# Performance work log

Hardware: AMD Instinct MI355X
Metric: run time of the kernel (lower is better)

## Reference

```python
import jax, jax.numpy as jnp
from jax import lax
import numpy as np

B, L, H, T = 64, 512, 768, 9


def setup_inputs() -> dict:
    key = jax.random.key(0)
    ks = jax.random.split(key, 6)
    hidden = jax.random.normal(ks[0], (B, L, H), dtype=jnp.float32)
    attention_mask = jnp.ones((B, L), dtype=jnp.int32)
    labels = jax.random.randint(ks[1], (B, L), 0, T).astype(jnp.int64)
    W = jax.random.normal(ks[2], (H, T), dtype=jnp.float32) * 0.02
    b = jnp.zeros((T,), dtype=jnp.float32)
    start_trans = jax.random.normal(ks[3], (T,), dtype=jnp.float32) * 0.1
    end_trans = jax.random.normal(ks[4], (T,), dtype=jnp.float32) * 0.1
    trans = jax.random.normal(ks[5], (T, T), dtype=jnp.float32) * 0.1
    return {"hidden": hidden, "attention_mask": attention_mask, "labels": labels,
            "W": W, "b": b, "start_trans": start_trans, "end_trans": end_trans, "trans": trans}


def _crf_nll(logits, safe_labels, mask, start_trans, end_trans, trans):
    # torchcrf: llh = numerator(path score) - denominator(log partition); loss = -mean(llh)
    maskf = mask.astype(logits.dtype)  # [B,L]
    # ---- numerator (gold path score) ----
    first_tags = safe_labels[:, 0]  # [B]
    num = start_trans[first_tags] + jnp.take_along_axis(logits[:, 0], first_tags[:, None], axis=1)[:, 0]
    emit = jnp.take_along_axis(logits, safe_labels[..., None], axis=2)[..., 0]  # [B,L]
    step_trans = trans[safe_labels[:, :-1], safe_labels[:, 1:]]  # [B,L-1]
    num = num + jnp.sum((step_trans + emit[:, 1:]) * maskf[:, 1:], axis=1)
    seq_ends = mask.sum(axis=1).astype(jnp.int32) - 1  # [B]
    last_tags = jnp.take_along_axis(safe_labels, seq_ends[:, None], axis=1)[:, 0]
    num = num + end_trans[last_tags]
    # ---- denominator (forward algorithm, logsumexp recurrence) ----
    def step(score, inp):
        e_t, m_t = inp  # [B,T], [B] bool
        # broadcast: score[b,i] + trans[i,j] + e_t[b,j]
        nxt = jax.nn.logsumexp(score[:, :, None] + trans[None, :, :] + e_t[:, None, :], axis=1)
        score = jnp.where(m_t[:, None], nxt, score)
        return score, None

    init = start_trans[None, :] + logits[:, 0]  # [B,T]
    xs = (jnp.swapaxes(logits[:, 1:], 0, 1), jnp.swapaxes(mask[:, 1:], 0, 1))
    final, _ = lax.scan(step, init, xs)
    denom = jax.nn.logsumexp(final + end_trans[None, :], axis=1)  # [B]
    llh = num - denom
    return -jnp.mean(llh)


def reference(hidden, attention_mask, labels, W, b, start_trans, end_trans, trans):
    logits = hidden @ W + b  # [B,L,T]
    mask = attention_mask.astype(bool)
    safe_labels = jnp.where(labels == -100, 0, labels)
    loss = _crf_nll(logits, safe_labels, mask, start_trans, end_trans, trans)
    return loss, logits
```

## Files before the change

### kernel.cpp

```cpp
#include <hip/hip_runtime.h>
#include <hip/hip_bf16.h>

#define NB 64
#define NL 512
#define NH 768
#define NT 9

#define LOG2E 1.4426950408889634f
#define LN2   0.6931471805599453f
#define NEG_INF -1e30f

#if defined(__has_builtin)
#if __has_builtin(__builtin_amdgcn_exp2f)
#define EXP2F(x) __builtin_amdgcn_exp2f(x)
#else
#define EXP2F(x) exp2f(x)
#endif
#if __has_builtin(__builtin_amdgcn_logf)
#define LOG2F(x) __builtin_amdgcn_logf(x)
#else
#define LOG2F(x) log2f(x)
#endif
#else
#define EXP2F(x) exp2f(x)
#define LOG2F(x) log2f(x)
#endif

__global__ __launch_bounds__(256) void gemm_kernel(
    const float* __restrict__ hidden, const float* __restrict__ W,
    const float* __restrict__ bias, float* __restrict__ out)
{
  __shared__ __align__(16) float w_lds[4 * 192 * 12];
  const int tid = threadIdx.x;
  for (int idx = tid; idx < NH * NT; idx += 256) {
    int k = idx / NT;
    int j = idx - k * NT;
    w_lds[(k & 3) * 2304 + (k >> 2) * 12 + j] = W[idx];
  }
  if (blockIdx.x == 0 && tid == 0) out[0] = 0.0f;
  __syncthreads();

  const int lane = tid & 63;
  const int wave = tid >> 6;
  const int gw = blockIdx.x * 4 + wave;
  const float bj = (lane < NT) ? bias[lane] : 0.0f;

  for (int row = gw; row < NB * NL; row += 4096) {
    const float4* hp = reinterpret_cast<const float4*>(hidden + (size_t)row * NH);
    float acc[NT];
#pragma unroll
    for (int j = 0; j < NT; ++j) acc[j] = 0.0f;
#pragma unroll
    for (int i = 0; i < 3; ++i) {
      const int kk = lane + 64 * i;
      const float4 h4 = hp[kk];
#pragma unroll
      for (int m = 0; m < 4; ++m) {
        const float hh = (m == 0) ? h4.x : (m == 1) ? h4.y : (m == 2) ? h4.z : h4.w;
        const float* wl = &w_lds[m * 2304 + kk * 12];
        const float4 wa = *reinterpret_cast<const float4*>(wl);
        const float4 wb = *reinterpret_cast<const float4*>(wl + 4);
        const float w8 = wl[8];
        acc[0] = fmaf(hh, wa.x, acc[0]);
        acc[1] = fmaf(hh, wa.y, acc[1]);
        acc[2] = fmaf(hh, wa.z, acc[2]);
        acc[3] = fmaf(hh, wa.w, acc[3]);
        acc[4] = fmaf(hh, wb.x, acc[4]);
        acc[5] = fmaf(hh, wb.y, acc[5]);
        acc[6] = fmaf(hh, wb.z, acc[6]);
        acc[7] = fmaf(hh, wb.w, acc[7]);
        acc[8] = fmaf(hh, w8, acc[8]);
      }
    }
#pragma unroll
    for (int off = 32; off >= 1; off >>= 1) {
#pragma unroll
      for (int j = 0; j < NT; ++j) acc[j] += __shfl_xor(acc[j], off);
    }
    float v = acc[0];
#pragma unroll
    for (int j = 1; j < NT; ++j)
      if (lane == j) v = acc[j];
    if (lane < NT) out[1 + (size_t)row * NT + lane] = v + bj;
  }
}

#define NC 32
#define CS 16

__global__ __launch_bounds__(576) void crf_kernel(
    const float* __restrict__ logits,
    const int* __restrict__ mask, const int* __restrict__ labels,
    const float* __restrict__ start_trans, const float* __restrict__ end_trans,
    const float* __restrict__ trans, float* __restrict__ loss_out)
{
  const int b = blockIdx.x;
  const int tid = threadIdx.x;

  __shared__ float lg[NL * NT];
  __shared__ float trans_s[NT * NT];
  __shared__ float E_s[NT * NT];
  __shared__ int mask_s[NL];
  __shared__ float P[NC * NT * NT];
  __shared__ float red_num[9];
  __shared__ float red_cnt[9];

  const float* lgg = logits + (size_t)b * NL * NT;
  for (int idx = tid; idx < NL * NT; idx += 576) lg[idx] = lgg[idx];
  if (tid < NT * NT) {
    float tv = trans[tid];
    trans_s[tid] = tv;
    E_s[tid] = EXP2F(tv * LOG2E);
  }
  if (tid < NL) mask_s[tid] = mask[b * NL + tid];
  __syncthreads();

  float numpart = 0.0f, cntpart = 0.0f;
  if (tid < NL) {
    int lab = labels[b * NL + tid];
    if (lab == -100) lab = 0;
    if (tid == 0) {
      numpart = start_trans[lab] + lg[lab];
    } else {
      int labp = labels[b * NL + tid - 1];
      if (labp == -100) labp = 0;
      float mf = (float)mask_s[tid];
      numpart = mf * (trans_s[labp * NT + lab] + lg[tid * NT + lab]);
    }
    cntpart = (float)mask_s[tid];
  }
#pragma unroll
  for (int off = 32; off >= 1; off >>= 1) {
    numpart += __shfl_down(numpart, off);
    cntpart += __shfl_down(cntpart, off);
  }
  if ((tid & 63) == 0) {
    red_num[tid >> 6] = numpart;
    red_cnt[tid >> 6] = cntpart;
  }

  if (tid < NC * NT) {
    const int c = tid / NT;
    const int i = tid - c * NT;
    float Er[NT * NT];
#pragma unroll
    for (int kj = 0; kj < NT * NT; ++kj) Er[kj] = E_s[kj];
    float run[NT];
    const int t0 = 1 + CS * c;
    if (mask_s[t0]) {
#pragma unroll
      for (int j = 0; j < NT; ++j) run[j] = trans_s[i * NT + j] + lg[t0 * NT + j];
    } else {
#pragma unroll
      for (int j = 0; j < NT; ++j) run[j] = (i == j) ? 0.0f : NEG_INF;
    }
    const int tend = min(t0 + CS, NL);
    for (int t = t0 + 1; t < tend; ++t) {
      if (!mask_s[t]) continue;
      float m = run[0];
#pragma unroll
      for (int k = 1; k < NT; ++k) m = fmaxf(m, run[k]);
      float p[NT];
#pragma unroll
      for (int k = 0; k < NT; ++k) p[k] = EXP2F((run[k] - m) * LOG2E);
      float dot[NT];
#pragma unroll
      for (int j = 0; j < NT; ++j) dot[j] = 0.0f;
#pragma unroll
      for (int k = 0; k < NT; ++k) {
#pragma unroll
        for (int j = 0; j < NT; ++j) dot[j] = fmaf(p[k], Er[k * NT + j], dot[j]);
      }
#pragma unroll
      for (int j = 0; j < NT; ++j)
        run[j] = fmaf(LOG2F(dot[j]), LN2, m) + lg[t * NT + j];
    }
#pragma unroll
    for (int j = 0; j < NT; ++j) P[c * (NT * NT) + i * NT + j] = run[j];
  }
  __syncthreads();

  if (tid < 64) {
    const int j = tid;
    const int jj = (j < NT) ? j : 0;
    float v = (j < NT) ? (start_trans[j] + lg[j]) : NEG_INF;
    for (int c = 0; c < NC; ++c) {
      float s[NT];
#pragma unroll
      for (int i = 0; i < NT; ++i)
        s[i] = __shfl(v, i) + P[c * (NT * NT) + i * NT + jj];
      float m = s[0];
#pragma unroll
      for (int i = 1; i < NT; ++i) m = fmaxf(m, s[i]);
      float sum = 0.0f;
#pragma unroll
      for (int i = 0; i < NT; ++i) sum += EXP2F((s[i] - m) * LOG2E);
      v = fmaf(LOG2F(sum), LN2, m);
    }
    float x = (j < NT) ? (v + end_trans[j]) : NEG_INF;
    float m = x;
#pragma unroll
    for (int off = 32; off >= 1; off >>= 1) m = fmaxf(m, __shfl_xor(m, off));
    float e = (j < NT) ? EXP2F((x - m) * LOG2E) : 0.0f;
#pragma unroll
    for (int off = 32; off >= 1; off >>= 1) e += __shfl_xor(e, off);
    if (tid == 0) {
      float denom = fmaf(LOG2F(e), LN2, m);
      float num = 0.0f, cnt = 0.0f;
#pragma unroll
      for (int w = 0; w < 9; ++w) {
        num += red_num[w];
        cnt += red_cnt[w];
      }
      int seq_end = (int)cnt - 1;
      int lastlab = labels[b * NL + seq_end];
      if (lastlab == -100) lastlab = 0;
      num += end_trans[lastlab];
      float llh = num - denom;
      atomicAdd(loss_out, -llh * (1.0f / NB));
    }
  }
}

extern "C" void kernel_launch(void* const* d_in, const int* in_sizes, int n_in,
                              void* d_out, int out_size, void* d_ws, size_t ws_size,
                              hipStream_t stream) {
  const float* hidden      = (const float*)d_in[0];
  const int*   attn_mask   = (const int*)d_in[1];
  const int*   labels      = (const int*)d_in[2];
  const float* W           = (const float*)d_in[3];
  const float* bias        = (const float*)d_in[4];
  const float* start_trans = (const float*)d_in[5];
  const float* end_trans   = (const float*)d_in[6];
  const float* trans       = (const float*)d_in[7];
  float* out = (float*)d_out;

  hipLaunchKernelGGL(gemm_kernel, dim3(1024), dim3(256), 0, stream,
                     hidden, W, bias, out);
  hipLaunchKernelGGL(crf_kernel, dim3(64), dim3(576), 0, stream,
                     out + 1, attn_mask, labels, start_trans, end_trans, trans, out);
}
```

Before: 187.3 us.

## Cache W in registers, process two rows per wave, vectorize CRF logits load

The GEMM kernel now preloads each lane's slice of W into 108 registers and processes two hidden rows per wave iteration, splitting the final cross-lane reduction so the two half-waves finish different rows. This removes repeated LDS reads of W and halves the shuffle-reduction cost per row. Logits are also written to an aligned workspace so the CRF kernel can load them with float4 vector loads instead of unaligned scalar loads. The large register footprint may lower occupancy, and the extra workspace store adds write traffic.

New measurement: 189.0 us. No clear change (+0.9%).

```diff
diff --git a/kernel.cpp b/kernel.cpp
--- a/kernel.cpp
+++ b/kernel.cpp
@@ -28,60 +28,86 @@
 
 __global__ __launch_bounds__(256) void gemm_kernel(
     const float* __restrict__ hidden, const float* __restrict__ W,
-    const float* __restrict__ bias, float* __restrict__ out)
+    const float* __restrict__ bias, float* __restrict__ out,
+    float* __restrict__ ws)
 {
-  __shared__ __align__(16) float w_lds[4 * 192 * 12];
+  __shared__ __align__(16) float w_lds[NH * NT];
   const int tid = threadIdx.x;
-  for (int idx = tid; idx < NH * NT; idx += 256) {
-    int k = idx / NT;
-    int j = idx - k * NT;
-    w_lds[(k & 3) * 2304 + (k >> 2) * 12 + j] = W[idx];
-  }
+  for (int idx = tid; idx < NH * NT / 4; idx += 256)
+    reinterpret_cast<float4*>(w_lds)[idx] = reinterpret_cast<const float4*>(W)[idx];
   if (blockIdx.x == 0 && tid == 0) out[0] = 0.0f;
   __syncthreads();
 
   const int lane = tid & 63;
-  const int wave = tid >> 6;
-  const int gw = blockIdx.x * 4 + wave;
-  const float bj = (lane < NT) ? bias[lane] : 0.0f;
-
-  for (int row = gw; row < NB * NL; row += 4096) {
-    const float4* hp = reinterpret_cast<const float4*>(hidden + (size_t)row * NH);
-    float acc[NT];
-#pragma unroll
-    for (int j = 0; j < NT; ++j) acc[j] = 0.0f;
+  const int wv = blockIdx.x * 4 + (tid >> 6);
+  const int jj = (lane < 32) ? lane : lane - 32;
+  const float bx = (jj < NT) ? bias[jj] : 0.0f;
+
+  float wreg[3][4][NT];
+#pragma unroll
+  for (int i = 0; i < 3; ++i) {
+#pragma unroll
+    for (int m = 0; m < 4; ++m) {
+      const float* wl = &w_lds[(4 * (lane + 64 * i) + m) * NT];
+#pragma unroll
+      for (int j = 0; j < NT; ++j) wreg[i][m][j] = wl[j];
+    }
+  }
+
+  for (int p = wv; p < NB * NL / 2; p += 4096) {
+    const float4* hp0 = reinterpret_cast<const float4*>(hidden + (size_t)(2 * p) * NH);
+    const float4* hp1 = reinterpret_cast<const float4*>(hidden + (size_t)(2 * p + 1) * NH);
+    float4 a[3], b[3];
+#pragma unroll
+    for (int i = 0; i < 3; ++i) a[i] = hp0[lane + 64 * i];
+#pragma unroll
+    for (int i = 0; i < 3; ++i) b[i] = hp1[lane + 64 * i];
+
+    float acc0[NT], acc1[NT];
+#pragma unroll
+    for (int j = 0; j < NT; ++j) { acc0[j] = 0.0f; acc1[j] = 0.0f; }
 #pragma unroll
     for (int i = 0; i < 3; ++i) {
-      const int kk = lane + 64 * i;
-      const float4 h4 = hp[kk];
 #pragma unroll
       for (int m = 0; m < 4; ++m) {
-        const float hh = (m == 0) ? h4.x : (m == 1) ? h4.y : (m == 2) ? h4.z : h4.w;
-        const float* wl = &w_lds[m * 2304 + kk * 12];
-        const float4 wa = *reinterpret_cast<const float4*>(wl);
-        const float4 wb = *reinterpret_cast<const float4*>(wl + 4);
-        const float w8 = wl[8];
-        acc[0] = fmaf(hh, wa.x, acc[0]);
-        acc[1] = fmaf(hh, wa.y, acc[1]);
-        acc[2] = fmaf(hh, wa.z, acc[2]);
-        acc[3] = fmaf(hh, wa.w, acc[3]);
-        acc[4] = fmaf(hh, wb.x, acc[4]);
-        acc[5] = fmaf(hh, wb.y, acc[5]);
-        acc[6] = fmaf(hh, wb.z, acc[6]);
-        acc[7] = fmaf(hh, wb.w, acc[7]);
-        acc[8] = fmaf(hh, w8, acc[8]);
-      }
-    }
-#pragma unroll
-    for (int off = 32; off >= 1; off >>= 1) {
-#pragma unroll
-      for (int j = 0; j < NT; ++j) acc[j] += __shfl_xor(acc[j], off);
-    }
-    float v = acc[0];
+        const float ha = (m == 0) ? a[i].x : (m == 1) ? a[i].y : (m == 2) ? a[i].z : a[i].w;
+        const float hb = (m == 0) ? b[i].x : (m == 1) ? b[i].y : (m == 2) ? b[i].z : b[i].w;
+#pragma unroll
+        for (int j = 0; j < NT; ++j) {
+          acc0[j] = fmaf(ha, wreg[i][m][j], acc0[j]);
+          acc1[j] = fmaf(hb, wreg[i][m][j], acc1[j]);
+        }
+      }
+    }
+#pragma unroll
+    for (int off = 1; off <= 16; off <<= 1) {
+#pragma unroll
+      for (int j = 0; j < NT; ++j) {
+        acc0[j] += __shfl_xor(acc0[j], off);
+        acc1[j] += __shfl_xor(acc1[j], off);
+      }
+    }
+    float tot[NT];
+#pragma unroll
+    for (int j = 0; j < NT; ++j) {
+      const float xsel = (lane < 32) ? acc1[j] : acc0[j];
+      const float other = __shfl_xor(xsel, 32);
+      tot[j] = ((lane < 32) ? acc0[j] : acc1[j]) + other;
+    }
+    float v = tot[0];
 #pragma unroll
     for (int j = 1; j < NT; ++j)
-      if (lane == j) v = acc[j];
-    if (lane < NT) out[1 + (size_t)row * NT + lane] = v + bj;
+      if (jj == j) v = tot[j];
+    v += bx;
+    if (lane < NT) {
+      const size_t o = (size_t)(2 * p) * NT + jj;
+      out[1 + o] = v;
+      ws[o] = v;
+    } else if (lane >= 32 && jj < NT) {
+      const size_t o = (size_t)(2 * p + 1) * NT + jj;
+      out[1 + o] = v;
+      ws[o] = v;
+    }
   }
 }
 
@@ -89,7 +115,7 @@
 #define CS 16
 
 __global__ __launch_bounds__(576) void crf_kernel(
-    const float* __restrict__ logits,
+    const float* __restrict__ logits_ws,
     const int* __restrict__ mask, const int* __restrict__ labels,
     const float* __restrict__ start_trans, const float* __restrict__ end_trans,
     const float* __restrict__ trans, float* __restrict__ loss_out)
@@ -97,7 +123,7 @@
   const int b = blockIdx.x;
   const int tid = threadIdx.x;
 
-  __shared__ float lg[NL * NT];
+  __shared__ __align__(16) float lg[NL * NT];
   __shared__ float trans_s[NT * NT];
   __shared__ float E_s[NT * NT];
   __shared__ int mask_s[NL];
@@ -105,8 +131,10 @@
   __shared__ float red_num[9];
   __shared__ float red_cnt[9];
 
-  const float* lgg = logits + (size_t)b * NL * NT;
-  for (int idx = tid; idx < NL * NT; idx += 576) lg[idx] = lgg[idx];
+  const float4* lgg4 = reinterpret_cast<const float4*>(logits_ws + (size_t)b * NL * NT);
+#pragma unroll
+  for (int r = 0; r < 2; ++r)
+    reinterpret_cast<float4*>(lg)[tid + 576 * r] = lgg4[tid + 576 * r];
   if (tid < NT * NT) {
     float tv = trans[tid];
     trans_s[tid] = tv;
@@ -234,9 +262,10 @@
   const float* end_trans   = (const float*)d_in[6];
   const float* trans       = (const float*)d_in[7];
   float* out = (float*)d_out;
+  float* ws  = (float*)d_ws;
 
   hipLaunchKernelGGL(gemm_kernel, dim3(1024), dim3(256), 0, stream,
-                     hidden, W, bias, out);
+                     hidden, W, bias, out, ws);
   hipLaunchKernelGGL(crf_kernel, dim3(64), dim3(576), 0, stream,
-                     out + 1, attn_mask, labels, start_trans, end_trans, trans, out);
+                     ws, attn_mask, labels, start_trans, end_trans, trans, out);
 }
```
